# Kernel tuning notes

Measured on AMD Instinct MI355X. Metric: run time of the kernel, lower is better.

The kernel has to match this reference:

```python
import jax, jax.numpy as jnp
import numpy as np

N_NODES = 10000
N_EDGES = 320000
D = 256
L = 3
BN_EPS = 1e-5


def _segment_softmax(logits, seg, num_segments):
    # numerically stable softmax over variable-sized segments (incoming edges per node)
    m = jax.ops.segment_max(logits, seg, num_segments=num_segments)
    e = jnp.exp(logits - m[seg])
    s = jax.ops.segment_sum(e, seg, num_segments=num_segments)
    return e / s[seg]


def setup_inputs() -> dict:
    key = jax.random.key(0)
    ks = jax.random.split(key, 20)
    scale = 1.0 / np.sqrt(D)
    inp = {
        "x": jax.random.normal(ks[0], (N_NODES, D), dtype=jnp.float32),
        "edge_index": jax.random.randint(ks[1], (2, N_EDGES), 0, N_NODES, dtype=jnp.int64),
        # TransformerConv params (heads=1, concat=False)
        "Wq": jax.random.normal(ks[2], (D, D), jnp.float32) * scale,
        "bq": jnp.zeros((D,), jnp.float32),
        "Wk": jax.random.normal(ks[3], (D, D), jnp.float32) * scale,
        "bk": jnp.zeros((D,), jnp.float32),
        "Wv": jax.random.normal(ks[4], (D, D), jnp.float32) * scale,
        "bv": jnp.zeros((D,), jnp.float32),
        "Ws": jax.random.normal(ks[5], (D, D), jnp.float32) * scale,  # lin_skip (root weight)
        "bs": jnp.zeros((D,), jnp.float32),
        # SAGEConv params per layer: lin_l (neighbors, with bias), lin_r (root, no bias)
        "Wl": jax.random.normal(ks[6], (L, D, D), jnp.float32) * scale,
        "bl": jnp.zeros((L, D), jnp.float32),
        "Wr": jax.random.normal(ks[7], (L, D, D), jnp.float32) * scale,
        # BatchNorm affine params (eval mode: running_mean=0, running_var=1)
        "gamma": jnp.ones((L, D), jnp.float32) + 0.1 * jax.random.normal(ks[8], (L, D), jnp.float32),
        "beta": 0.1 * jax.random.normal(ks[9], (L, D), jnp.float32),
        # residual gate parameter (scalar)
        "alpha_res": jnp.asarray(0.5, jnp.float32),
    }
    return inp


def reference(x, edge_index, Wq, bq, Wk, bk, Wv, bv, Ws, bs, Wl, bl, Wr, gamma, beta, alpha_res):
    src, dst = edge_index[0], edge_index[1]  # message j -> i
    n, d = x.shape

    # ---- TransformerConv (heads=1, concat=False, eval: no dropout) ----
    q = x @ Wq + bq
    k = x @ Wk + bk
    v = x @ Wv + bv
    logits = jnp.sum(q[dst] * k[src], axis=-1) / jnp.sqrt(jnp.asarray(d, x.dtype))  # [E]
    attn = _segment_softmax(logits, dst, n)  # [E]
    agg = jax.ops.segment_sum(attn[:, None] * v[src], dst, num_segments=n)  # [N,D]
    h = agg + x @ Ws + bs  # root/skip connection
    h = jax.nn.relu(h)

    # in-degree for SAGE mean aggregation
    deg = jax.ops.segment_sum(jnp.ones((src.shape[0],), x.dtype), dst, num_segments=n)
    deg = jnp.maximum(deg, 1.0)[:, None]

    prev = h
    bn_scale = 1.0 / jnp.sqrt(1.0 + BN_EPS)  # eval-mode BN with running stats (0, 1)
    al = jax.nn.sigmoid(alpha_res)
    for i in range(Wl.shape[0]):
        mean_nb = jax.ops.segment_sum(h[src], dst, num_segments=n) / deg  # gather-mean-scatter
        z = mean_nb @ Wl[i] + bl[i] + h @ Wr[i]
        z = z * bn_scale * gamma[i] + beta[i]
        z = al * z + (1.0 - al) * prev
        h = jax.nn.relu(z)
        prev = h
    return h
```

## Files before the change

kernel.cpp:

```cpp
#include <hip/hip_runtime.h>
#include <hip/hip_bf16.h>

typedef unsigned short u16;
typedef unsigned int u32;
typedef unsigned char u8;
typedef __bf16 bf16x8 __attribute__((ext_vector_type(8)));
typedef float f32x4 __attribute__((ext_vector_type(4)));
typedef float f32x2 __attribute__((ext_vector_type(2)));

#define DIM 256
#define BN_SCALE 0.9999950000374997f

__device__ __forceinline__ float bf2f(u16 u) {
    union { unsigned u; float f; } c; c.u = ((unsigned)u) << 16; return c.f;
}
__device__ __forceinline__ u16 f2bf(float f) {
    union { float f; unsigned u; } c; c.f = f;
    unsigned u = c.u;
    unsigned r = (u + 0x7FFFu + ((u >> 16) & 1u)) >> 16;
    return (u16)r;
}
__device__ __forceinline__ float asf(unsigned u) {
    union { unsigned u; float f; } c; c.u = u; return c.f;
}
__device__ __forceinline__ void cvt8(int4 v, float* f) {
    unsigned a0 = (unsigned)v.x, a1 = (unsigned)v.y, a2 = (unsigned)v.z, a3 = (unsigned)v.w;
    f[0] = asf(a0 << 16); f[1] = asf(a0 & 0xFFFF0000u);
    f[2] = asf(a1 << 16); f[3] = asf(a1 & 0xFFFF0000u);
    f[4] = asf(a2 << 16); f[5] = asf(a2 & 0xFFFF0000u);
    f[6] = asf(a3 << 16); f[7] = asf(a3 & 0xFFFF0000u);
}
__device__ __forceinline__ void dec4(unsigned u, float* f) {
    f32x2 lo = __builtin_amdgcn_cvt_pk_f32_fp8((int)u, false);
    f32x2 hi = __builtin_amdgcn_cvt_pk_f32_fp8((int)u, true);
    f[0] = lo.x; f[1] = lo.y; f[2] = hi.x; f[3] = hi.y;
}
__device__ __forceinline__ unsigned pack4(float a, float b, float c, float d) {
    int u = __builtin_amdgcn_cvt_pk_fp8_f32(a, b, 0, false);
    u = __builtin_amdgcn_cvt_pk_fp8_f32(c, d, u, true);
    return (unsigned)u;
}
__device__ __forceinline__ void gl_lds16(const u16* g, u16* l) {
    __builtin_amdgcn_global_load_lds(
        (__attribute__((address_space(1))) const u32*)(const void*)g,
        (__attribute__((address_space(3))) u32*)(void*)l, 16, 0, 0);
}

__device__ __forceinline__ int2 detect_inline(const u16* __restrict__ xu,
                                              const long long* __restrict__ e64) {
    int lane = threadIdx.x & 63;
    int pl = 0;
#pragma unroll
    for (int j = 0; j < 4; ++j) {
        u16 u = xu[lane * 4 + j];
        int ex = (u >> 7) & 0xFF;
        pl += (u == 0 || (ex >= 115 && ex <= 131)) ? 1 : 0;
    }
#pragma unroll
    for (int o = 32; o; o >>= 1) pl += __shfl_xor(pl, o, 64);
    long long hi = e64[lane] >> 32;
    unsigned long long b = __ballot(hi == 0);
    int2 r; r.x = (pl >= 200) ? 1 : 0; r.y = (b == ~0ULL) ? 1 : 0;
    return r;
}

struct CvtDesc { const void* src[9]; int cum[10]; };
__global__ void k_convert(CvtDesc d, const u16* __restrict__ xu,
                          const long long* __restrict__ e64,
                          u16* __restrict__ arena, int total,
                          int* __restrict__ deg, int N) {
    int2 fl = detect_inline(xu, e64);
    int i = blockIdx.x * 256 + threadIdx.x;
    if (i < N) deg[i] = 0;
    if (i >= total) return;
    int t = 0;
    while (i >= d.cum[t + 1]) ++t;
    int j = i - d.cum[t];
    u16 v;
    if (fl.x) v = ((const u16*)d.src[t])[j];
    else      v = f2bf(((const float*)d.src[t])[j]);
    arena[i] = v;
}

struct TDesc { const void* base[3]; int L; };
__global__ __launch_bounds__(256) void k_transpose(TDesc td, const void* w0,
                                                   const void* w1, const void* w2,
                                                   const void* w3,
                                                   const u16* __restrict__ xu,
                                                   const long long* __restrict__ e64,
                                                   u16* __restrict__ WT) {
    __shared__ u16 t[64][72];
    int2 fl = detect_inline(xu, e64);
    int m = blockIdx.x >> 4, tl = blockIdx.x & 15;
    int tr = (tl >> 2) * 64, tc = (tl & 3) * 64;
    const void* S;
    size_t eoff = 0;
    if (m < 4)            S = (m == 0) ? w0 : (m == 1) ? w1 : (m == 2) ? w2 : w3;
    else if (m < 4 + td.L) { S = td.base[1]; eoff = (size_t)(m - 4) * DIM * DIM; }
    else                   { S = td.base[2]; eoff = (size_t)(m - 4 - td.L) * DIM * DIM; }
    u16* D = WT + (size_t)m * DIM * DIM;
    int r = threadIdx.x >> 2, cs = (threadIdx.x & 3) * 16;
    size_t src_idx = eoff + (size_t)(tr + r) * 256 + tc + cs;
    if (fl.x) {
        const u16* S16 = (const u16*)S + src_idx;
        *(int4*)&t[r][cs]     = *(const int4*)S16;
        *(int4*)&t[r][cs + 8] = *(const int4*)(S16 + 8);
    } else {
        const float* SF = (const float*)S + src_idx;
        u16 tmp[16];
#pragma unroll
        for (int q = 0; q < 4; ++q) {
            float4 v = *(const float4*)(SF + q * 4);
            tmp[q * 4] = f2bf(v.x); tmp[q * 4 + 1] = f2bf(v.y);
            tmp[q * 4 + 2] = f2bf(v.z); tmp[q * 4 + 3] = f2bf(v.w);
        }
        *(int4*)&t[r][cs]     = *(const int4*)&tmp[0];
        *(int4*)&t[r][cs + 8] = *(const int4*)&tmp[8];
    }
    __syncthreads();
    u16 tmp[16];
#pragma unroll
    for (int j = 0; j < 16; ++j) tmp[j] = t[cs + j][r];
    *(int4*)&D[(tc + r) * 256 + tr + cs]     = *(int4*)&tmp[0];
    *(int4*)&D[(tc + r) * 256 + tr + cs + 8] = *(int4*)&tmp[8];
}

__global__ void k_edges(const int* __restrict__ ei32, const u16* __restrict__ xu,
                        int* __restrict__ deg, int E) {
    int2 fl = detect_inline(xu, (const long long*)ei32);
    int e = blockIdx.x * 256 + threadIdx.x;
    if (e >= E) return;
    const long long* ei64 = (const long long*)ei32;
    int d = fl.y ? (int)ei64[E + e] : ei32[E + e];
    atomicAdd(&deg[d], 1);
}

__global__ __launch_bounds__(1024) void k_scan(const int* __restrict__ deg,
                                               int* __restrict__ offs,
                                               int* __restrict__ cursor, int N, int E) {
    __shared__ int s[1024];
    int t = threadIdx.x;
    int P = (N + 1023) >> 10;
    int base = t * P;
    int run = 0;
    for (int j = 0; j < P; ++j) { int idx = base + j; if (idx < N) run += deg[idx]; }
    s[t] = run;
    __syncthreads();
    int total = run;
    for (int off = 1; off < 1024; off <<= 1) {
        int v = 0;
        if (t >= off) v = s[t - off];
        __syncthreads();
        if (t >= off) s[t] += v;
        __syncthreads();
    }
    int r = s[t] - total;
    for (int j = 0; j < P; ++j) {
        int idx = base + j;
        if (idx < N) { offs[idx] = r; cursor[idx] = r; r += deg[idx]; }
    }
    if (t == 0) offs[N] = E;
}

__global__ void k_fill(const int* __restrict__ ei32, const u16* __restrict__ xu,
                       int* __restrict__ cursor, int* __restrict__ csr, int E) {
    int2 fl = detect_inline(xu, (const long long*)ei32);
    int e = blockIdx.x * 256 + threadIdx.x;
    if (e >= E) return;
    const long long* ei64 = (const long long*)ei32;
    int s = fl.y ? (int)ei64[e]     : ei32[e];
    int d = fl.y ? (int)ei64[E + e] : ei32[E + e];
    int pos = atomicAdd(&cursor[d], 1);
    csr[pos] = s;
}

__global__ __launch_bounds__(256) void gemm_qkvs(
    const u16* __restrict__ x, const u16* __restrict__ WT,
    const u16* __restrict__ bias, u16* __restrict__ out,
    u8* __restrict__ kv8, int M) {
    __shared__ __align__(16) u16 lds[16384];
    u16* As = lds;
    u16* Bs = lds + 8192;
    int tid = threadIdx.x, w = tid >> 6, lane = tid & 63;
    int l15 = lane & 15, quad = lane >> 4;
    int lr = lane >> 3, lc = lane & 7;
    int bm0 = blockIdx.x * 128, bn0 = blockIdx.y * 128;
    f32x4 acc[4][4];
#pragma unroll
    for (int a = 0; a < 4; ++a)
#pragma unroll
        for (int b = 0; b < 4; ++b) acc[a][b] = (f32x4){0.f, 0.f, 0.f, 0.f};

    for (int k0 = 0; k0 < 256; k0 += 64) {
#pragma unroll
        for (int j = 0; j < 4; ++j) {
            int ar = (w * 4 + j) * 8 + lr;
            int grow = bm0 + ar; if (grow >= M) grow = M - 1;
            gl_lds16(x + (size_t)grow * 256 + k0 + lc * 8, &As[(w * 4 + j) * 512]);
        }
#pragma unroll
        for (int j = 0; j < 4; ++j) {
            int nr = (w * 4 + j) * 8 + lr;
            gl_lds16(WT + (size_t)(bn0 + nr) * 256 + k0 + lc * 8, &Bs[(w * 4 + j) * 512]);
        }
        __syncthreads();
        int wm = w & 1, wn = w >> 1;
#pragma unroll
        for (int s = 0; s < 2; ++s) {
            bf16x8 a[4], b[4];
#pragma unroll
            for (int t = 0; t < 4; ++t)
                a[t] = *(const bf16x8*)&As[(wm * 64 + t * 16 + l15) * 64 + s * 32 + quad * 8];
#pragma unroll
            for (int t = 0; t < 4; ++t)
                b[t] = *(const bf16x8*)&Bs[(wn * 64 + t * 16 + l15) * 64 + s * 32 + quad * 8];
#pragma unroll
            for (int rt = 0; rt < 4; ++rt)
#pragma unroll
                for (int ct = 0; ct < 4; ++ct)
                    acc[rt][ct] = __builtin_amdgcn_mfma_f32_16x16x32_bf16(a[rt], b[ct], acc[rt][ct], 0, 0, 0);
        }
        __syncthreads();
    }
    int wm = w & 1, wn = w >> 1;
    u16* oL = lds + w * 4096;
#pragma unroll
    for (int rt = 0; rt < 4; ++rt)
#pragma unroll
        for (int ct = 0; ct < 4; ++ct) {
            int col = bn0 + wn * 64 + ct * 16 + l15;
            float bv = bf2f(bias[col]);
#pragma unroll
            for (int r = 0; r < 4; ++r)
                oL[(rt * 16 + quad * 4 + r) * 64 + ct * 16 + l15] = f2bf(acc[rt][ct][r] + bv);
        }
    __syncthreads();
    int c0 = bn0 + wn * 64 + lc * 8;
#pragma unroll
    for (int j = 0; j < 8; ++j) {
        int orow = j * 8 + lr;
        int grow = bm0 + wm * 64 + orow;
        if (grow < M) {
            int4 hv = *(const int4*)&oL[orow * 64 + lc * 8];
            *(int4*)&out[(size_t)grow * 1024 + c0] = hv;
            if (c0 >= 256 && c0 < 768) {
                float f[8]; cvt8(hv, f);
                uint2 o8;
                o8.x = pack4(f[0], f[1], f[2], f[3]);
                o8.y = pack4(f[4], f[5], f[6], f[7]);
                *(uint2*)(kv8 + (size_t)grow * 512 + (c0 - 256)) = o8;
            }
        }
    }
}

__global__ __launch_bounds__(256) void k_attn(const u16* __restrict__ qkvs,
                                              const u8* __restrict__ kv8,
                                              const int* __restrict__ csr,
                                              const int* __restrict__ offs,
                                              u16* __restrict__ hb,
                                              u8* __restrict__ h8, int N) {
    int wv = threadIdx.x >> 6, lane = threadIdx.x & 63;
    int i = blockIdx.x * 4 + wv;
    if (i >= N) return;
    int sub = lane & 7, e8 = lane >> 3;
    size_t row = (size_t)i * 1024;

    float qf[32];
    {
        const u16* qp = qkvs + row + sub * 32;
#pragma unroll
        for (int j = 0; j < 4; ++j) {
            int4 v = *(const int4*)(qp + j * 8);
            float t[8]; cvt8(v, t);
#pragma unroll
            for (int d = 0; d < 8; ++d) qf[j * 8 + d] = t[d] * 0.0625f;
        }
    }
    int e0 = offs[i], e1 = offs[i + 1];
    float m = -1e30f, denom = 0.f;
    float acc[32];
#pragma unroll
    for (int j = 0; j < 32; ++j) acc[j] = 0.f;

    for (int base = e0; base < e1; base += 8) {
        int e = base + e8;
        int sidx = csr[(e < e1) ? e : (e1 - 1)];
        const u8* kp = kv8 + (size_t)sidx * 512 + sub * 32;
        uint4 ka = *(const uint4*)kp;
        uint4 kb = *(const uint4*)(kp + 16);
        uint4 va = *(const uint4*)(kp + 256);
        uint4 vb = *(const uint4*)(kp + 272);
        unsigned kw[8] = {ka.x, ka.y, ka.z, ka.w, kb.x, kb.y, kb.z, kb.w};
        float p = 0.f;
#pragma unroll
        for (int j = 0; j < 8; ++j) {
            float t[4]; dec4(kw[j], t);
            p += qf[j * 4] * t[0] + qf[j * 4 + 1] * t[1] + qf[j * 4 + 2] * t[2] + qf[j * 4 + 3] * t[3];
        }
        p += __shfl_xor(p, 1, 64);
        p += __shfl_xor(p, 2, 64);
        p += __shfl_xor(p, 4, 64);
        if (e >= e1) p = -1e30f;
        float pm = p;
        pm = fmaxf(pm, __shfl_xor(pm, 8, 64));
        pm = fmaxf(pm, __shfl_xor(pm, 16, 64));
        pm = fmaxf(pm, __shfl_xor(pm, 32, 64));
        if (pm > m) {
            float sc = __expf(m - pm);
            denom *= sc;
#pragma unroll
            for (int j = 0; j < 32; ++j) acc[j] *= sc;
            m = pm;
        }
        float w = __expf(p - m);
        denom += w;
        unsigned vw[8] = {va.x, va.y, va.z, va.w, vb.x, vb.y, vb.z, vb.w};
#pragma unroll
        for (int j = 0; j < 8; ++j) {
            float t[4]; dec4(vw[j], t);
            acc[j * 4]     += w * t[0];
            acc[j * 4 + 1] += w * t[1];
            acc[j * 4 + 2] += w * t[2];
            acc[j * 4 + 3] += w * t[3];
        }
    }
    denom += __shfl_xor(denom, 8, 64);
    denom += __shfl_xor(denom, 16, 64);
    denom += __shfl_xor(denom, 32, 64);
    float inv = (denom > 0.f) ? 1.f / denom : 0.f;
#pragma unroll
    for (int j = 0; j < 32; ++j) {
        acc[j] += __shfl_xor(acc[j], 8, 64);
        acc[j] += __shfl_xor(acc[j], 16, 64);
        acc[j] += __shfl_xor(acc[j], 32, 64);
    }
    if (e8 == 0) {
        const u16* skp = qkvs + row + 768 + sub * 32;
        float h[32];
#pragma unroll
        for (int j = 0; j < 4; ++j) {
            int4 sv = *(const int4*)(skp + j * 8);
            float t[8]; cvt8(sv, t);
            u16 o[8];
#pragma unroll
            for (int d = 0; d < 8; ++d) {
                float hv = fmaxf(acc[j * 8 + d] * inv + t[d], 0.f);
                h[j * 8 + d] = hv;
                o[d] = f2bf(hv);
            }
            *(int4*)(hb + (size_t)i * 256 + sub * 32 + j * 8) = *(const int4*)o;
        }
        uint4 p0, p1;
        p0.x = pack4(h[0], h[1], h[2], h[3]);   p0.y = pack4(h[4], h[5], h[6], h[7]);
        p0.z = pack4(h[8], h[9], h[10], h[11]); p0.w = pack4(h[12], h[13], h[14], h[15]);
        p1.x = pack4(h[16], h[17], h[18], h[19]); p1.y = pack4(h[20], h[21], h[22], h[23]);
        p1.z = pack4(h[24], h[25], h[26], h[27]); p1.w = pack4(h[28], h[29], h[30], h[31]);
        *(uint4*)(h8 + (size_t)i * 256 + sub * 32) = p0;
        *(uint4*)(h8 + (size_t)i * 256 + sub * 32 + 16) = p1;
    }
}

__global__ __launch_bounds__(256) void k_agg(const u8* __restrict__ h8,
                                             const int* __restrict__ csr,
                                             const int* __restrict__ offs,
                                             u16* __restrict__ mean_out, int N) {
    int w = threadIdx.x >> 6, lane = threadIdx.x & 63;
    int i = blockIdx.x * 4 + w;
    if (i >= N) return;
    int g = lane >> 4, sub = lane & 15;
    int e0 = offs[i], e1 = offs[i + 1];
    float acc[16];
#pragma unroll
    for (int d = 0; d < 16; ++d) acc[d] = 0.f;
    int e = e0;
    for (; e + 8 <= e1; e += 8) {
        int s0 = csr[e + g], s1 = csr[e + 4 + g];
        uint4 r0 = *(const uint4*)(h8 + (size_t)s0 * 256 + sub * 16);
        uint4 r1 = *(const uint4*)(h8 + (size_t)s1 * 256 + sub * 16);
        float f0[16], f1[16];
        dec4(r0.x, f0); dec4(r0.y, f0 + 4); dec4(r0.z, f0 + 8); dec4(r0.w, f0 + 12);
        dec4(r1.x, f1); dec4(r1.y, f1 + 4); dec4(r1.z, f1 + 8); dec4(r1.w, f1 + 12);
#pragma unroll
        for (int d = 0; d < 16; ++d) acc[d] += f0[d] + f1[d];
    }
    for (; e + 4 <= e1; e += 4) {
        int s0 = csr[e + g];
        uint4 r0 = *(const uint4*)(h8 + (size_t)s0 * 256 + sub * 16);
        float f0[16];
        dec4(r0.x, f0); dec4(r0.y, f0 + 4); dec4(r0.z, f0 + 8); dec4(r0.w, f0 + 12);
#pragma unroll
        for (int d = 0; d < 16; ++d) acc[d] += f0[d];
    }
    if (e + g < e1) {
        int s0 = csr[e + g];
        uint4 r0 = *(const uint4*)(h8 + (size_t)s0 * 256 + sub * 16);
        float f0[16];
        dec4(r0.x, f0); dec4(r0.y, f0 + 4); dec4(r0.z, f0 + 8); dec4(r0.w, f0 + 12);
#pragma unroll
        for (int d = 0; d < 16; ++d) acc[d] += f0[d];
    }
#pragma unroll
    for (int d = 0; d < 16; ++d) {
        acc[d] += __shfl_xor(acc[d], 16, 64);
        acc[d] += __shfl_xor(acc[d], 32, 64);
    }
    if (g == 0) {
        int dg = e1 - e0; if (dg < 1) dg = 1;
        float inv = 1.f / (float)dg;
        u16 o16[16];
#pragma unroll
        for (int d = 0; d < 16; ++d) o16[d] = f2bf(acc[d] * inv);
        u16* dst = mean_out + (size_t)i * 256 + sub * 16;
        *(int4*)dst = *(const int4*)&o16[0];
        *(int4*)(dst + 8) = *(const int4*)&o16[8];
    }
}

__global__ __launch_bounds__(256) void gemm_sage(
    const u16* __restrict__ meanA, const u16* __restrict__ hin,
    const u16* __restrict__ WlT, const u16* __restrict__ WrT,
    const u16* __restrict__ bl, const u16* __restrict__ gamma,
    const u16* __restrict__ beta, const u16* __restrict__ alpha,
    u16* __restrict__ hout, u8* __restrict__ h8out, float* __restrict__ fout, int M) {
    __shared__ __align__(16) u16 lds[12288];
    u16* As = lds;
    u16* Bs = lds + 8192;
    int tid = threadIdx.x, w = tid >> 6, lane = tid & 63;
    int l15 = lane & 15, quad = lane >> 4;
    int lr = lane >> 3, lc = lane & 7;
    int bm0 = blockIdx.x * 128, n0 = blockIdx.y * 64;
    f32x4 acc[2][4];
#pragma unroll
    for (int a = 0; a < 2; ++a)
#pragma unroll
        for (int b = 0; b < 4; ++b) acc[a][b] = (f32x4){0.f, 0.f, 0.f, 0.f};

    for (int k0 = 0; k0 < 512; k0 += 64) {
        const u16* Asrc = (k0 < 256) ? meanA : hin;
        const u16* Bsrc = (k0 < 256) ? WlT : WrT;
        int kc = k0 & 255;
#pragma unroll
        for (int j = 0; j < 4; ++j) {
            int ar = (w * 4 + j) * 8 + lr;
            int grow = bm0 + ar; if (grow >= M) grow = M - 1;
            gl_lds16(Asrc + (size_t)grow * 256 + kc + lc * 8, &As[(w * 4 + j) * 512]);
        }
#pragma unroll
        for (int j = 0; j < 2; ++j) {
            int nr = (w * 2 + j) * 8 + lr;
            gl_lds16(Bsrc + (size_t)(n0 + nr) * 256 + kc + lc * 8, &Bs[(w * 2 + j) * 512]);
        }
        __syncthreads();
#pragma unroll
        for (int s = 0; s < 2; ++s) {
            bf16x8 a[2], b[4];
#pragma unroll
            for (int t = 0; t < 2; ++t)
                a[t] = *(const bf16x8*)&As[(w * 32 + t * 16 + l15) * 64 + s * 32 + quad * 8];
#pragma unroll
            for (int t = 0; t < 4; ++t)
                b[t] = *(const bf16x8*)&Bs[(t * 16 + l15) * 64 + s * 32 + quad * 8];
#pragma unroll
            for (int rt = 0; rt < 2; ++rt)
#pragma unroll
                for (int ct = 0; ct < 4; ++ct)
                    acc[rt][ct] = __builtin_amdgcn_mfma_f32_16x16x32_bf16(a[rt], b[ct], acc[rt][ct], 0, 0, 0);
        }
        __syncthreads();
    }

    float al = 1.f / (1.f + __expf(-bf2f(alpha[0])));
    float alc = 1.f - al;
    u16* oL = lds + w * 2048;
#pragma unroll
    for (int rt = 0; rt < 2; ++rt)
#pragma unroll
        for (int ct = 0; ct < 4; ++ct) {
            int col = n0 + ct * 16 + l15;
            float g  = bf2f(gamma[col]) * BN_SCALE;
            float be = bf2f(beta[col]);
            float bb = bf2f(bl[col]);
#pragma unroll
            for (int r = 0; r < 4; ++r) {
                int grow = bm0 + w * 32 + rt * 16 + quad * 4 + r;
                float z = (acc[rt][ct][r] + bb) * g + be;
                float prev = (grow < M) ? bf2f(hin[(size_t)grow * 256 + col]) : 0.f;
                z = al * z + alc * prev;
                z = fmaxf(z, 0.f);
                oL[(rt * 16 + quad * 4 + r) * 64 + ct * 16 + l15] = f2bf(z);
                if (fout && grow < M) fout[(size_t)grow * 256 + col] = z;
            }
        }
    if (!hout) return;
    __syncthreads();
#pragma unroll
    for (int j = 0; j < 4; ++j) {
        int orow = j * 8 + lr;
        int grow = bm0 + w * 32 + orow;
        if (grow < M) {
            int4 hv = *(const int4*)&oL[orow * 64 + lc * 8];
            *(int4*)&hout[(size_t)grow * 256 + n0 + lc * 8] = hv;
            float f[8]; cvt8(hv, f);
            uint2 o8;
            o8.x = pack4(f[0], f[1], f[2], f[3]);
            o8.y = pack4(f[4], f[5], f[6], f[7]);
            *(uint2*)(h8out + (size_t)grow * 256 + n0 + lc * 8) = o8;
        }
    }
}

extern "C" void kernel_launch(void* const* d_in, const int* in_sizes, int n_in,
                              void* d_out, int out_size, void* d_ws, size_t ws_size,
                              hipStream_t stream) {
    int N = in_sizes[0] / DIM;
    int E = in_sizes[1] / 2;
    int L = in_sizes[10] / (DIM * DIM);

    const u16* xu = (const u16*)d_in[0];
    const long long* e64 = (const long long*)d_in[1];

    const int map9[9] = {0, 3, 5, 7, 9, 11, 13, 14, 15};
    CvtDesc cd;
    cd.cum[0] = 0;
    for (int t = 0; t < 9; ++t) {
        cd.src[t] = d_in[map9[t]];
        cd.cum[t + 1] = cd.cum[t] + in_sizes[map9[t]];
    }
    int total = cd.cum[9];

    char* ws = (char*)d_ws;
    size_t off = 0;
    auto take = [&](size_t bytes) { size_t c = off; off = (off + bytes + 255) & ~255ULL; return c; };

    u16* arena  = (u16*)(ws + take((size_t)total * 2));
    u16* WT     = (u16*)(ws + take((size_t)(4 + 2 * L) * DIM * DIM * 2));
    int* csr    = (int*)(ws + take((size_t)E * 4));
    int* deg    = (int*)(ws + take((size_t)N * 4));
    int* offs   = (int*)(ws + take((size_t)(N + 1) * 4));
    int* cursor = (int*)(ws + take((size_t)N * 4));
    u16* hB0    = (u16*)(ws + take((size_t)N * DIM * 2));
    u8*  kv8    = (u8*)(ws + take((size_t)N * 512));
    u8*  h8     = (u8*)(ws + take((size_t)N * 256));
    u16* qkvsB  = (u16*)(ws + take((size_t)N * 1024 * 2));
    u16* meanB  = qkvsB;
    u16* hB1    = qkvsB + (size_t)N * DIM;
    (void)ws_size; (void)n_in; (void)out_size;

    const u16* xb    = arena + cd.cum[0];
    const u16* biasF = arena + cd.cum[1];
    const u16* blb   = arena + cd.cum[5];
    const u16* gmb   = arena + cd.cum[6];
    const u16* btb   = arena + cd.cum[7];
    const u16* alb   = arena + cd.cum[8];

    k_convert<<<(total + 255) / 256, 256, 0, stream>>>(cd, xu, e64, arena, total, deg, N);

    TDesc td;
    td.base[0] = nullptr; td.base[1] = d_in[10]; td.base[2] = d_in[12]; td.L = L;
    k_transpose<<<(4 + 2 * L) * 16, 256, 0, stream>>>(td, d_in[2], d_in[4], d_in[6], d_in[8],
                                                      xu, e64, WT);

    int eb = (E + 255) / 256;
    k_edges<<<eb, 256, 0, stream>>>((const int*)d_in[1], xu, deg, E);
    k_scan<<<1, 1024, 0, stream>>>(deg, offs, cursor, N, E);
    k_fill<<<eb, 256, 0, stream>>>((const int*)d_in[1], xu, cursor, csr, E);

    int Mb128 = (N + 127) / 128;
    gemm_qkvs<<<dim3(Mb128, 8), 256, 0, stream>>>(xb, WT, biasF, qkvsB, kv8, N);
    k_attn<<<(N + 3) / 4, 256, 0, stream>>>(qkvsB, kv8, csr, offs, hB0, h8, N);

    for (int l = 0; l < L; ++l) {
        const u16* hin = (l & 1) ? hB1 : hB0;
        u16* hout      = (l == L - 1) ? nullptr : ((l & 1) ? hB0 : hB1);
        u8*  h8o       = (l == L - 1) ? nullptr : h8;
        float* fout    = (l == L - 1) ? (float*)d_out : nullptr;
        k_agg<<<(N + 3) / 4, 256, 0, stream>>>(h8, csr, offs, meanB, N);
        gemm_sage<<<dim3(Mb128, 4), 256, 0, stream>>>(
            meanB, hin, WT + (size_t)(4 + l) * DIM * DIM, WT + (size_t)(4 + L + l) * DIM * DIM,
            blb + (size_t)l * DIM, gmb + (size_t)l * DIM, btb + (size_t)l * DIM,
            alb, hout, h8o, fout, N);
    }
}
```

Baseline: 293.1 us.

## Fuse convert, transpose and degree-count kernels; skip bf16 K/V writes

Merges the input conversion, weight transpose and in-degree counting into one prep kernel that dispatches on block index, and replaces the deg zeroing with hipMemsetAsync. This removes two kernel launches and their serial dependencies. The QKVS GEMM no longer writes the bf16 K and V columns, which only the fp8 copy consumes. Q and skip are stored in a compact 512-wide buffer, cutting global write traffic. The degree atomics now run in the same launch as the other prep work and rely on the memset finishing first, which stream order guarantees.

```diff
diff --git a/kernel.cpp b/kernel.cpp
--- a/kernel.cpp
+++ b/kernel.cpp
@@ -65,74 +65,66 @@
 }
 
 struct CvtDesc { const void* src[9]; int cum[10]; };
-__global__ void k_convert(CvtDesc d, const u16* __restrict__ xu,
-                          const long long* __restrict__ e64,
-                          u16* __restrict__ arena, int total,
-                          int* __restrict__ deg, int N) {
-    int2 fl = detect_inline(xu, e64);
-    int i = blockIdx.x * 256 + threadIdx.x;
-    if (i < N) deg[i] = 0;
-    if (i >= total) return;
-    int t = 0;
-    while (i >= d.cum[t + 1]) ++t;
-    int j = i - d.cum[t];
-    u16 v;
-    if (fl.x) v = ((const u16*)d.src[t])[j];
-    else      v = f2bf(((const float*)d.src[t])[j]);
-    arena[i] = v;
-}
-
-struct TDesc { const void* base[3]; int L; };
-__global__ __launch_bounds__(256) void k_transpose(TDesc td, const void* w0,
-                                                   const void* w1, const void* w2,
-                                                   const void* w3,
-                                                   const u16* __restrict__ xu,
-                                                   const long long* __restrict__ e64,
-                                                   u16* __restrict__ WT) {
+struct TDesc { const void* baseL; const void* baseR; int L; };
+__global__ __launch_bounds__(256) void k_prep(
+    CvtDesc cd, TDesc td, const void* w0, const void* w1, const void* w2, const void* w3,
+    const u16* __restrict__ xu, const long long* __restrict__ e64,
+    const int* __restrict__ ei32, int E,
+    u16* __restrict__ arena, int total, int* __restrict__ deg,
+    u16* __restrict__ WT, int Tblocks, int Cblocks) {
     __shared__ u16 t[64][72];
     int2 fl = detect_inline(xu, e64);
-    int m = blockIdx.x >> 4, tl = blockIdx.x & 15;
-    int tr = (tl >> 2) * 64, tc = (tl & 3) * 64;
-    const void* S;
-    size_t eoff = 0;
-    if (m < 4)            S = (m == 0) ? w0 : (m == 1) ? w1 : (m == 2) ? w2 : w3;
-    else if (m < 4 + td.L) { S = td.base[1]; eoff = (size_t)(m - 4) * DIM * DIM; }
-    else                   { S = td.base[2]; eoff = (size_t)(m - 4 - td.L) * DIM * DIM; }
-    u16* D = WT + (size_t)m * DIM * DIM;
-    int r = threadIdx.x >> 2, cs = (threadIdx.x & 3) * 16;
-    size_t src_idx = eoff + (size_t)(tr + r) * 256 + tc + cs;
-    if (fl.x) {
-        const u16* S16 = (const u16*)S + src_idx;
-        *(int4*)&t[r][cs]     = *(const int4*)S16;
-        *(int4*)&t[r][cs + 8] = *(const int4*)(S16 + 8);
+    int bx = (int)blockIdx.x;
+    if (bx < Tblocks) {
+        int m = bx >> 4, tl = bx & 15;
+        int tr = (tl >> 2) * 64, tc = (tl & 3) * 64;
+        const void* S;
+        size_t eoff = 0;
+        if (m < 4)             S = (m == 0) ? w0 : (m == 1) ? w1 : (m == 2) ? w2 : w3;
+        else if (m < 4 + td.L) { S = td.baseL; eoff = (size_t)(m - 4) * DIM * DIM; }
+        else                   { S = td.baseR; eoff = (size_t)(m - 4 - td.L) * DIM * DIM; }
+        u16* D = WT + (size_t)m * DIM * DIM;
+        int r = threadIdx.x >> 2, cs = (threadIdx.x & 3) * 16;
+        size_t src_idx = eoff + (size_t)(tr + r) * 256 + tc + cs;
+        if (fl.x) {
+            const u16* S16 = (const u16*)S + src_idx;
+            *(int4*)&t[r][cs]     = *(const int4*)S16;
+            *(int4*)&t[r][cs + 8] = *(const int4*)(S16 + 8);
+        } else {
+            const float* SF = (const float*)S + src_idx;
+            u16 tmp[16];
+#pragma unroll
+            for (int q = 0; q < 4; ++q) {
+                float4 v = *(const float4*)(SF + q * 4);
+                tmp[q * 4] = f2bf(v.x); tmp[q * 4 + 1] = f2bf(v.y);
+                tmp[q * 4 + 2] = f2bf(v.z); tmp[q * 4 + 3] = f2bf(v.w);
+            }
+            *(int4*)&t[r][cs]     = *(const int4*)&tmp[0];
+            *(int4*)&t[r][cs + 8] = *(const int4*)&tmp[8];
+        }
+        __syncthreads();
+        u16 tmp[16];
+#pragma unroll
+        for (int j = 0; j < 16; ++j) tmp[j] = t[cs + j][r];
+        *(int4*)&D[(tc + r) * 256 + tr + cs]     = *(int4*)&tmp[0];
+        *(int4*)&D[(tc + r) * 256 + tr + cs + 8] = *(int4*)&tmp[8];
+    } else if (bx < Tblocks + Cblocks) {
+        int i = (bx - Tblocks) * 256 + threadIdx.x;
+        if (i >= total) return;
+        int t2 = 0;
+        while (i >= cd.cum[t2 + 1]) ++t2;
+        int j = i - cd.cum[t2];
+        u16 v;
+        if (fl.x) v = ((const u16*)cd.src[t2])[j];
+        else      v = f2bf(((const float*)cd.src[t2])[j]);
+        arena[i] = v;
     } else {
-        const float* SF = (const float*)S + src_idx;
-        u16 tmp[16];
-#pragma unroll
-        for (int q = 0; q < 4; ++q) {
-            float4 v = *(const float4*)(SF + q * 4);
-            tmp[q * 4] = f2bf(v.x); tmp[q * 4 + 1] = f2bf(v.y);
-            tmp[q * 4 + 2] = f2bf(v.z); tmp[q * 4 + 3] = f2bf(v.w);
-        }
-        *(int4*)&t[r][cs]     = *(const int4*)&tmp[0];
-        *(int4*)&t[r][cs + 8] = *(const int4*)&tmp[8];
-    }
-    __syncthreads();
-    u16 tmp[16];
-#pragma unroll
-    for (int j = 0; j < 16; ++j) tmp[j] = t[cs + j][r];
-    *(int4*)&D[(tc + r) * 256 + tr + cs]     = *(int4*)&tmp[0];
-    *(int4*)&D[(tc + r) * 256 + tr + cs + 8] = *(int4*)&tmp[8];
-}
-
-__global__ void k_edges(const int* __restrict__ ei32, const u16* __restrict__ xu,
-                        int* __restrict__ deg, int E) {
-    int2 fl = detect_inline(xu, (const long long*)ei32);
-    int e = blockIdx.x * 256 + threadIdx.x;
-    if (e >= E) return;
-    const long long* ei64 = (const long long*)ei32;
-    int d = fl.y ? (int)ei64[E + e] : ei32[E + e];
-    atomicAdd(&deg[d], 1);
+        int e = (bx - Tblocks - Cblocks) * 256 + threadIdx.x;
+        if (e >= E) return;
+        const long long* ei64 = (const long long*)ei32;
+        int d = fl.y ? (int)ei64[E + e] : ei32[E + e];
+        atomicAdd(&deg[d], 1);
+    }
 }
 
 __global__ __launch_bounds__(1024) void k_scan(const int* __restrict__ deg,
@@ -176,7 +168,7 @@
 
 __global__ __launch_bounds__(256) void gemm_qkvs(
     const u16* __restrict__ x, const u16* __restrict__ WT,
-    const u16* __restrict__ bias, u16* __restrict__ out,
+    const u16* __restrict__ bias, u16* __restrict__ qs,
     u8* __restrict__ kv8, int M) {
     __shared__ __align__(16) u16 lds[16384];
     u16* As = lds;
@@ -242,19 +234,22 @@
         int grow = bm0 + wm * 64 + orow;
         if (grow < M) {
             int4 hv = *(const int4*)&oL[orow * 64 + lc * 8];
-            *(int4*)&out[(size_t)grow * 1024 + c0] = hv;
-            if (c0 >= 256 && c0 < 768) {
+            if (c0 < 256) {
+                *(int4*)&qs[(size_t)grow * 512 + c0] = hv;
+            } else if (c0 < 768) {
                 float f[8]; cvt8(hv, f);
                 uint2 o8;
                 o8.x = pack4(f[0], f[1], f[2], f[3]);
                 o8.y = pack4(f[4], f[5], f[6], f[7]);
                 *(uint2*)(kv8 + (size_t)grow * 512 + (c0 - 256)) = o8;
+            } else {
+                *(int4*)&qs[(size_t)grow * 512 + (c0 - 512)] = hv;
             }
         }
     }
 }
 
-__global__ __launch_bounds__(256) void k_attn(const u16* __restrict__ qkvs,
+__global__ __launch_bounds__(256) void k_attn(const u16* __restrict__ qs,
                                               const u8* __restrict__ kv8,
                                               const int* __restrict__ csr,
                                               const int* __restrict__ offs,
@@ -264,11 +259,11 @@
     int i = blockIdx.x * 4 + wv;
     if (i >= N) return;
     int sub = lane & 7, e8 = lane >> 3;
-    size_t row = (size_t)i * 1024;
+    size_t row = (size_t)i * 512;
 
     float qf[32];
     {
-        const u16* qp = qkvs + row + sub * 32;
+        const u16* qp = qs + row + sub * 32;
 #pragma unroll
         for (int j = 0; j < 4; ++j) {
             int4 v = *(const int4*)(qp + j * 8);
@@ -336,7 +331,7 @@
         acc[j] += __shfl_xor(acc[j], 32, 64);
     }
     if (e8 == 0) {
-        const u16* skp = qkvs + row + 768 + sub * 32;
+        const u16* skp = qs + row + 256 + sub * 32;
         float h[32];
 #pragma unroll
         for (int j = 0; j < 4; ++j) {
@@ -542,9 +537,9 @@
     u16* hB0    = (u16*)(ws + take((size_t)N * DIM * 2));
     u8*  kv8    = (u8*)(ws + take((size_t)N * 512));
     u8*  h8     = (u8*)(ws + take((size_t)N * 256));
-    u16* qkvsB  = (u16*)(ws + take((size_t)N * 1024 * 2));
-    u16* meanB  = qkvsB;
-    u16* hB1    = qkvsB + (size_t)N * DIM;
+    u16* qs     = (u16*)(ws + take((size_t)N * 512 * 2));
+    u16* meanB  = qs;
+    u16* hB1    = qs + (size_t)N * DIM;
     (void)ws_size; (void)n_in; (void)out_size;
 
     const u16* xb    = arena + cd.cum[0];
@@ -554,21 +549,23 @@
     const u16* btb   = arena + cd.cum[7];
     const u16* alb   = arena + cd.cum[8];
 
-    k_convert<<<(total + 255) / 256, 256, 0, stream>>>(cd, xu, e64, arena, total, deg, N);
+    hipMemsetAsync(deg, 0, (size_t)N * 4, stream);
 
     TDesc td;
-    td.base[0] = nullptr; td.base[1] = d_in[10]; td.base[2] = d_in[12]; td.L = L;
-    k_transpose<<<(4 + 2 * L) * 16, 256, 0, stream>>>(td, d_in[2], d_in[4], d_in[6], d_in[8],
-                                                      xu, e64, WT);
-
-    int eb = (E + 255) / 256;
-    k_edges<<<eb, 256, 0, stream>>>((const int*)d_in[1], xu, deg, E);
+    td.baseL = d_in[10]; td.baseR = d_in[12]; td.L = L;
+    int Tblocks = (4 + 2 * L) * 16;
+    int Cblocks = (total + 255) / 256;
+    int Eblocks = (E + 255) / 256;
+    k_prep<<<Tblocks + Cblocks + Eblocks, 256, 0, stream>>>(
+        cd, td, d_in[2], d_in[4], d_in[6], d_in[8], xu, e64,
+        (const int*)d_in[1], E, arena, total, deg, WT, Tblocks, Cblocks);
+
     k_scan<<<1, 1024, 0, stream>>>(deg, offs, cursor, N, E);
-    k_fill<<<eb, 256, 0, stream>>>((const int*)d_in[1], xu, cursor, csr, E);
+    k_fill<<<Eblocks, 256, 0, stream>>>((const int*)d_in[1], xu, cursor, csr, E);
 
     int Mb128 = (N + 127) / 128;
-    gemm_qkvs<<<dim3(Mb128, 8), 256, 0, stream>>>(xb, WT, biasF, qkvsB, kv8, N);
-    k_attn<<<(N + 3) / 4, 256, 0, stream>>>(qkvsB, kv8, csr, offs, hB0, h8, N);
+    gemm_qkvs<<<dim3(Mb128, 8), 256, 0, stream>>>(xb, WT, biasF, qs, kv8, N);
+    k_attn<<<(N + 3) / 4, 256, 0, stream>>>(qs, kv8, csr, offs, hB0, h8, N);
 
     for (int l = 0; l < L; ++l) {
         const u16* hin = (l & 1) ? hB1 : hB0;
```

Measured after the change: 289.5 us. Within noise of the previous version (-1.2%).
